# Performance work log

Hardware: AMD Instinct MI355X
Metric: run time of the kernel (lower is better)

The kernel has to match this reference:

```python
import jax, jax.numpy as jnp
import numpy as np

B = 32       # batch (number of packed sequences)
H = 16       # heads
E = 64       # embed per head
S = 512      # maxseqlen
SEQLEN = np.array([256 + (i * 37) % 257 for i in range(B)], dtype=np.int64)
NTOKENS = int(SEQLEN.sum())            # 11638
SCALE = 1.0 / np.sqrt(E)               # scale=True -> 1/sqrt(embed)

# host-side index construction for the ragged layout (seqlen is static config)
_b_tok = np.repeat(np.arange(B), SEQLEN)
_p_tok = np.concatenate([np.arange(L) for L in SEQLEN])
# flat gather indices into padded scores [B,H,S,S] for the packed ragged output,
# per-sample layout [H, L, L] contiguous
_out_idx = np.concatenate([
    (((b * H + np.arange(H)[:, None, None]) * S + np.arange(L)[None, :, None]) * S
     + np.arange(L)[None, None, :]).ravel()
    for b, L in enumerate(SEQLEN)
])


def setup_inputs() -> dict:
    key = jax.random.key(0)
    k1, k2 = jax.random.split(key)
    batch1 = jax.random.normal(k1, (NTOKENS, H * E), dtype=jnp.float32)
    batch2 = jax.random.normal(k2, (NTOKENS, H * E), dtype=jnp.float32)
    seqlen = jnp.asarray(SEQLEN)
    return {"batch1": batch1, "batch2": batch2, "batch": B, "seqlen": seqlen}


def reference(batch1, batch2, batch, seqlen):
    # scatter packed tokens into zero-padded [B, S, H, E]
    q = jnp.zeros((B, S, H, E), batch1.dtype).at[_b_tok, _p_tok].set(batch1.reshape(-1, H, E))
    k = jnp.zeros((B, S, H, E), batch2.dtype).at[_b_tok, _p_tok].set(batch2.reshape(-1, H, E))
    # per-sample, per-head QK^T with scale: [B, H, S, S]
    scores = jnp.einsum('bqhe,bkhe->bhqk', q, k) * jnp.asarray(SCALE, batch1.dtype)
    # gather ragged valid blocks -> flat [sum_b H*L_b*L_b]
    return scores.reshape(-1)[jnp.asarray(_out_idx)]
```

## Files before the change

kernel.cpp:

```cpp
#include <hip/hip_runtime.h>
#include <hip/hip_bf16.h>
#include <stdint.h>

#define NH 16
#define NE 64
#define BT 128
#define QK_SCALE 0.125f

typedef __attribute__((ext_vector_type(8))) short short8;
typedef __attribute__((ext_vector_type(16))) float f32x16;
typedef __attribute__((ext_vector_type(4))) float float4v;


__device__ __forceinline__ short8 lds_frag(const unsigned char* base, int row, int e0) {
    int off = row * 128 + e0 * 2;
    off ^= (row & 7) << 4;
    return *reinterpret_cast<const short8*>(base + off);
}

__global__ __launch_bounds__(256, 2)
void bmm1_kernel(const float* __restrict__ Qg, const float* __restrict__ Kg,
                 float* __restrict__ out)
{
    __shared__ __align__(16) unsigned char lds[65536];

    const int b  = blockIdx.z;
    const int h  = blockIdx.y;
    const int tq = blockIdx.x >> 2;
    const int tk = blockIdx.x & 3;
    const int L  = 256 + (b * 37) % 257;
    if (tq * BT >= L || tk * BT >= L) return;

    long long toff = 0, ooff = 0;
    for (int i = 0; i < b; ++i) {
        int Li = 256 + (i * 37) % 257;
        toff += Li;
        ooff += (long long)NH * Li * Li;
    }

    const int tid = threadIdx.x;

    const float* srcs[2] = {Qg, Kg};
    const int    t0s[2]  = {tq * BT, tk * BT};
    #pragma unroll
    for (int s = 0; s < 2; ++s) {
        const float* src = srcs[s];
        const int t0 = t0s[s];
        unsigned char* hibase = lds + s * 32768;
        unsigned char* lobase = hibase + 16384;
        #pragma unroll
        for (int it = 0; it < 8; ++it) {
            int r  = (tid >> 4) + it * 16;
            int rr = t0 + r;
            if (rr >= L) rr = L - 1;
            const float4v v = *reinterpret_cast<const float4v*>(
                src + (size_t)(toff + rr) * (NH * NE) + h * NE + (tid & 15) * 4);
            unsigned int hp[2], lp[2];
            #pragma unroll
            for (int j = 0; j < 2; ++j) {
                unsigned short hb[2], lb[2];
                #pragma unroll
                for (int jj = 0; jj < 2; ++jj) {
                    float x = v[j * 2 + jj];
                    __hip_bfloat16 hh = __float2bfloat16(x);
                    unsigned short us;
                    __builtin_memcpy(&us, &hh, 2);
                    hb[jj] = us;
                    float resid = x - __bfloat162float(hh);
                    __hip_bfloat16 ll = __float2bfloat16(resid);
                    __builtin_memcpy(&us, &ll, 2);
                    lb[jj] = us;
                }
                hp[j] = (unsigned int)hb[0] | ((unsigned int)hb[1] << 16);
                lp[j] = (unsigned int)lb[0] | ((unsigned int)lb[1] << 16);
            }
            int boff = r * 128 + (tid & 15) * 8;
            boff ^= (r & 7) << 4;
            *reinterpret_cast<uint2*>(hibase + boff) = make_uint2(hp[0], hp[1]);
            *reinterpret_cast<uint2*>(lobase + boff) = make_uint2(lp[0], lp[1]);
        }
    }
    __syncthreads();

    const int lane  = tid & 63;
    const int wave  = tid >> 6;
    const int wm    = wave >> 1, wn = wave & 1;
    const int rlane = lane & 31;
    const int klane = lane >> 5;

    const unsigned char* QH = lds;
    const unsigned char* QL = lds + 16384;
    const unsigned char* KH = lds + 32768;
    const unsigned char* KL = lds + 49152;

    f32x16 acc[2][2];
    #pragma unroll
    for (int mb = 0; mb < 2; ++mb)
        #pragma unroll
        for (int nb = 0; nb < 2; ++nb)
            acc[mb][nb] = (f32x16)0.0f;

    #pragma unroll
    for (int ec = 0; ec < 4; ++ec) {
        const int e0 = ec * 16 + klane * 8;
        short8 ah[2], al[2], bh[2], bl[2];
        #pragma unroll
        for (int mb = 0; mb < 2; ++mb) {
            int row = wm * 64 + mb * 32 + rlane;
            ah[mb] = lds_frag(QH, row, e0);
            al[mb] = lds_frag(QL, row, e0);
        }
        #pragma unroll
        for (int nb = 0; nb < 2; ++nb) {
            int row = wn * 64 + nb * 32 + rlane;
            bh[nb] = lds_frag(KH, row, e0);
            bl[nb] = lds_frag(KL, row, e0);
        }
        #pragma unroll
        for (int mb = 0; mb < 2; ++mb)
            #pragma unroll
            for (int nb = 0; nb < 2; ++nb) {
                acc[mb][nb] = __builtin_amdgcn_mfma_f32_32x32x16_bf16(ah[mb], bh[nb], acc[mb][nb], 0, 0, 0);
                acc[mb][nb] = __builtin_amdgcn_mfma_f32_32x32x16_bf16(ah[mb], bl[nb], acc[mb][nb], 0, 0, 0);
                acc[mb][nb] = __builtin_amdgcn_mfma_f32_32x32x16_bf16(al[mb], bh[nb], acc[mb][nb], 0, 0, 0);
            }
    }

    float* obase = out + ooff + (long long)h * L * L;
    #pragma unroll
    for (int mb = 0; mb < 2; ++mb) {
        #pragma unroll
        for (int nb = 0; nb < 2; ++nb) {
            int colg = tk * BT + wn * 64 + nb * 32 + rlane;
            if (colg >= L) continue;
            #pragma unroll
            for (int r = 0; r < 16; ++r) {
                int rowl = (r & 3) + 8 * (r >> 2) + 4 * klane;
                int rowg = tq * BT + wm * 64 + mb * 32 + rowl;
                if (rowg < L)
                    obase[(long long)rowg * L + colg] = acc[mb][nb][r] * QK_SCALE;
            }
        }
    }
}

extern "C" void kernel_launch(void* const* d_in, const int* in_sizes, int n_in,
                              void* d_out, int out_size, void* d_ws, size_t ws_size,
                              hipStream_t stream) {
    const float* Qg = (const float*)d_in[0];
    const float* Kg = (const float*)d_in[1];
    float* out = (float*)d_out;
    dim3 grid(16, NH, 32);
    bmm1_kernel<<<grid, 256, 0, stream>>>(Qg, Kg, out);
}
```

Measured before the change: 442.6 us.

## Use 512-thread blocks with smaller per-wave tiles and swizzled block order

Doubles threads per block to 512, so each wave computes a 32x64 output strip instead of 64x64. This halves accumulator registers and raises the launch-bounds occupancy target. The block index is remapped so consecutive blocks cover different (batch, head) pairs, and the scale is folded into Q before the bf16 split. Interior tiles also take a store path without bounds checks. Risks: 64KB of LDS per block may still cap residency, and scaling before splitting changes rounding slightly.

```diff
diff --git a/kernel.cpp b/kernel.cpp
--- a/kernel.cpp
+++ b/kernel.cpp
@@ -5,7 +5,6 @@
 #define NH 16
 #define NE 64
 #define BT 128
-#define QK_SCALE 0.125f
 
 typedef __attribute__((ext_vector_type(8))) short short8;
 typedef __attribute__((ext_vector_type(16))) float f32x16;
@@ -18,17 +17,21 @@
     return *reinterpret_cast<const short8*>(base + off);
 }
 
-__global__ __launch_bounds__(256, 2)
+__global__ __launch_bounds__(512, 4)
 void bmm1_kernel(const float* __restrict__ Qg, const float* __restrict__ Kg,
                  float* __restrict__ out)
 {
     __shared__ __align__(16) unsigned char lds[65536];
 
-    const int b  = blockIdx.z;
-    const int h  = blockIdx.y;
-    const int tq = blockIdx.x >> 2;
-    const int tk = blockIdx.x & 3;
-    const int L  = 256 + (b * 37) % 257;
+    const int l  = blockIdx.x + 16 * blockIdx.y + 256 * blockIdx.z;
+    const int r8 = l & 7;
+    const int g  = l >> 3;
+    const int p  = r8 + 8 * (g >> 4);
+    const int t  = g & 15;
+    const int b  = p >> 4, h = p & 15;
+    const int tq = t >> 2, tk = t & 3;
+
+    const int L = 256 + (b * 37) % 257;
     if (tq * BT >= L || tk * BT >= L) return;
 
     long long toff = 0, ooff = 0;
@@ -42,15 +45,17 @@
 
     const float* srcs[2] = {Qg, Kg};
     const int    t0s[2]  = {tq * BT, tk * BT};
+    const float  scl[2]  = {0.125f, 1.0f};
     #pragma unroll
     for (int s = 0; s < 2; ++s) {
         const float* src = srcs[s];
         const int t0 = t0s[s];
+        const float sc = scl[s];
         unsigned char* hibase = lds + s * 32768;
         unsigned char* lobase = hibase + 16384;
         #pragma unroll
-        for (int it = 0; it < 8; ++it) {
-            int r  = (tid >> 4) + it * 16;
+        for (int it = 0; it < 4; ++it) {
+            int r  = (tid >> 4) + it * 32;
             int rr = t0 + r;
             if (rr >= L) rr = L - 1;
             const float4v v = *reinterpret_cast<const float4v*>(
@@ -61,7 +66,7 @@
                 unsigned short hb[2], lb[2];
                 #pragma unroll
                 for (int jj = 0; jj < 2; ++jj) {
-                    float x = v[j * 2 + jj];
+                    float x = v[j * 2 + jj] * sc;
                     __hip_bfloat16 hh = __float2bfloat16(x);
                     unsigned short us;
                     __builtin_memcpy(&us, &hh, 2);
@@ -84,7 +89,8 @@
 
     const int lane  = tid & 63;
     const int wave  = tid >> 6;
-    const int wm    = wave >> 1, wn = wave & 1;
+    const int wm    = wave >> 1;
+    const int wn    = wave & 1;
     const int rlane = lane & 31;
     const int klane = lane >> 5;
 
@@ -93,52 +99,53 @@
     const unsigned char* KH = lds + 32768;
     const unsigned char* KL = lds + 49152;
 
-    f32x16 acc[2][2];
-    #pragma unroll
-    for (int mb = 0; mb < 2; ++mb)
-        #pragma unroll
-        for (int nb = 0; nb < 2; ++nb)
-            acc[mb][nb] = (f32x16)0.0f;
+    f32x16 acc[2];
+    acc[0] = (f32x16)0.0f;
+    acc[1] = (f32x16)0.0f;
 
     #pragma unroll
     for (int ec = 0; ec < 4; ++ec) {
         const int e0 = ec * 16 + klane * 8;
-        short8 ah[2], al[2], bh[2], bl[2];
-        #pragma unroll
-        for (int mb = 0; mb < 2; ++mb) {
-            int row = wm * 64 + mb * 32 + rlane;
-            ah[mb] = lds_frag(QH, row, e0);
-            al[mb] = lds_frag(QL, row, e0);
-        }
+        const int arow = wm * 32 + rlane;
+        short8 ah = lds_frag(QH, arow, e0);
+        short8 al = lds_frag(QL, arow, e0);
         #pragma unroll
         for (int nb = 0; nb < 2; ++nb) {
-            int row = wn * 64 + nb * 32 + rlane;
-            bh[nb] = lds_frag(KH, row, e0);
-            bl[nb] = lds_frag(KL, row, e0);
+            const int brow = wn * 64 + nb * 32 + rlane;
+            short8 bh = lds_frag(KH, brow, e0);
+            short8 bl = lds_frag(KL, brow, e0);
+            acc[nb] = __builtin_amdgcn_mfma_f32_32x32x16_bf16(ah, bh, acc[nb], 0, 0, 0);
+            acc[nb] = __builtin_amdgcn_mfma_f32_32x32x16_bf16(ah, bl, acc[nb], 0, 0, 0);
+            acc[nb] = __builtin_amdgcn_mfma_f32_32x32x16_bf16(al, bh, acc[nb], 0, 0, 0);
         }
-        #pragma unroll
-        for (int mb = 0; mb < 2; ++mb)
-            #pragma unroll
-            for (int nb = 0; nb < 2; ++nb) {
-                acc[mb][nb] = __builtin_amdgcn_mfma_f32_32x32x16_bf16(ah[mb], bh[nb], acc[mb][nb], 0, 0, 0);
-                acc[mb][nb] = __builtin_amdgcn_mfma_f32_32x32x16_bf16(ah[mb], bl[nb], acc[mb][nb], 0, 0, 0);
-                acc[mb][nb] = __builtin_amdgcn_mfma_f32_32x32x16_bf16(al[mb], bh[nb], acc[mb][nb], 0, 0, 0);
-            }
     }
 
+    const long long LL = L;
     float* obase = out + ooff + (long long)h * L * L;
-    #pragma unroll
-    for (int mb = 0; mb < 2; ++mb) {
+    const int row0 = tq * BT + wm * 32 + 4 * klane;
+    const bool interior = (tq * BT + BT <= L) && (tk * BT + BT <= L);
+
+    if (interior) {
         #pragma unroll
         for (int nb = 0; nb < 2; ++nb) {
-            int colg = tk * BT + wn * 64 + nb * 32 + rlane;
+            const int colg = tk * BT + wn * 64 + nb * 32 + rlane;
+            float* rp = obase + (long long)row0 * LL + colg;
+            #pragma unroll
+            for (int rr = 0; rr < 16; ++rr) {
+                const int c = (rr & 3) + 8 * (rr >> 2);
+                rp[(long long)c * LL] = acc[nb][rr];
+            }
+        }
+    } else {
+        #pragma unroll
+        for (int nb = 0; nb < 2; ++nb) {
+            const int colg = tk * BT + wn * 64 + nb * 32 + rlane;
             if (colg >= L) continue;
             #pragma unroll
-            for (int r = 0; r < 16; ++r) {
-                int rowl = (r & 3) + 8 * (r >> 2) + 4 * klane;
-                int rowg = tq * BT + wm * 64 + mb * 32 + rowl;
+            for (int rr = 0; rr < 16; ++rr) {
+                const int rowg = row0 + (rr & 3) + 8 * (rr >> 2);
                 if (rowg < L)
-                    obase[(long long)rowg * L + colg] = acc[mb][nb][r] * QK_SCALE;
+                    obase[(long long)rowg * LL + colg] = acc[nb][rr];
             }
         }
     }
@@ -151,5 +158,5 @@
     const float* Kg = (const float*)d_in[1];
     float* out = (float*)d_out;
     dim3 grid(16, NH, 32);
-    bmm1_kernel<<<grid, 256, 0, stream>>>(Qg, Kg, out);
+    bmm1_kernel<<<grid, 512, 0, stream>>>(Qg, Kg, out);
 }
```

New measurement: 382.7 us. 13.5% less time.
